# Optimization experiments

Measured on AMD Instinct MI355X. Metric: run time of the kernel, lower is better.

Reference implementation:

```python
import jax, jax.numpy as jnp
import numpy as np
import math

B_ = 4
L_ = 2048
D_MODEL = 1024
D_STATE = 128
D_CONV = 4
HEADDIM = 64
CHUNK = 256
D_INNER = 2 * D_MODEL
NHEADS = D_INNER // HEADDIM
CONV_DIM = D_INNER + 2 * D_STATE
D_IN_PROJ = 2 * D_INNER + 2 * D_STATE + NHEADS


def setup_inputs() -> dict:
    key = jax.random.key(0)
    ks = jax.random.split(key, 8)
    u = jax.random.normal(ks[0], (B_, L_, D_MODEL), jnp.float32)
    W_in = jax.random.normal(ks[1], (D_IN_PROJ, D_MODEL), jnp.float32) * 0.02
    conv_w = jax.random.normal(ks[2], (CONV_DIM, D_CONV), jnp.float32) * 0.2
    conv_b = jnp.zeros((CONV_DIM,), jnp.float32)
    # dt init as in the torch module: dt ~ logU(0.001, 0.1), inverse-softplus
    dt = jnp.exp(jax.random.uniform(ks[3], (NHEADS,), jnp.float32) * (math.log(0.1) - math.log(0.001)) + math.log(0.001))
    dt = jnp.clip(dt, 1e-4, None)
    dt_bias = dt + jnp.log(-jnp.expm1(-dt))
    A_log = jnp.log(jax.random.uniform(ks[4], (NHEADS,), jnp.float32, minval=1.0, maxval=1.1))
    D_param = jnp.ones((NHEADS,), jnp.float32)
    norm_w = jnp.ones((D_INNER,), jnp.float32)
    W_out = jax.random.normal(ks[5], (D_MODEL, D_INNER), jnp.float32) * 0.02
    return {"u": u, "W_in": W_in, "conv_w": conv_w, "conv_b": conv_b,
            "dt_bias": dt_bias, "A_log": A_log, "D_param": D_param,
            "norm_w": norm_w, "W_out": W_out}


def _ssd(x, dt, A, Bm, Cm):
    """Chunked SSD scan (mamba_chunk_scan_combined math, ngroups=1).
    x: (b,l,h,p)  dt: (b,l,h) post-softplus  A: (h,)  Bm/Cm: (b,l,n)."""
    b, l, h, p = x.shape
    n = Bm.shape[-1]
    nc = l // CHUNK
    xr = x.reshape(b, nc, CHUNK, h, p)
    dtr = dt.reshape(b, nc, CHUNK, h)
    Br = Bm.reshape(b, nc, CHUNK, n)
    Cr = Cm.reshape(b, nc, CHUNK, n)
    dA = dtr * A                                    # (b,nc,cs,h), negative
    dA_cs = jnp.cumsum(dA, axis=2)                  # (b,nc,cs,h)
    # intra-chunk decay L[i,j] = exp(sum_{k=j+1..i} dA_k) for i >= j else 0
    diff = dA_cs[:, :, :, None, :] - dA_cs[:, :, None, :, :]  # (b,nc,i,j,h)
    mask = jnp.tril(jnp.ones((CHUNK, CHUNK), bool))
    Lmat = jnp.exp(jnp.where(mask[None, None, :, :, None], diff, -jnp.inf))
    dtx = dtr[..., None] * xr                       # (b,nc,cs,h,p)
    Y_diag = jnp.einsum('bcin,bcjn,bcijh,bcjhp->bcihp', Cr, Br, Lmat, dtx)
    # per-chunk final states
    decay_states = jnp.exp(dA_cs[:, :, -1:, :] - dA_cs)  # (b,nc,cs,h)
    states = jnp.einsum('bcjn,bcjh,bcjhp->bchpn', Br, decay_states, dtx)
    # inter-chunk recurrence over nc
    chunk_decay = jnp.exp(dA_cs[:, :, -1, :])       # (b,nc,h)
    def step(carry, inp):
        s, d = inp
        return carry * d[:, :, None, None] + s, carry
    init = jnp.zeros((b, h, p, n), x.dtype)
    _, prev = jax.lax.scan(step, init, (jnp.moveaxis(states, 1, 0), jnp.moveaxis(chunk_decay, 1, 0)))
    prev = jnp.moveaxis(prev, 0, 1)                 # (b,nc,h,p,n): state entering each chunk
    Y_off = jnp.einsum('bcin,bchpn,bcih->bcihp', Cr, prev, jnp.exp(dA_cs))
    return (Y_diag + Y_off).reshape(b, l, h, p)


def reference(u, W_in, conv_w, conv_b, dt_bias, A_log, D_param, norm_w, W_out):
    b, l, _ = u.shape
    zxbcdt = jnp.einsum('bld,ed->ble', u, W_in)     # (b,l,d_in_proj)
    z = zxbcdt[..., :D_INNER]
    xBC = zxbcdt[..., D_INNER:D_INNER + CONV_DIM]
    dt = zxbcdt[..., D_INNER + CONV_DIM:]
    # depthwise causal conv1d + SiLU
    xt = jnp.moveaxis(xBC, 1, 2)                    # (b,c,l)
    y = jax.lax.conv_general_dilated(xt, conv_w[:, None, :], (1,), [(D_CONV - 1, 0)], feature_group_count=CONV_DIM)
    xBC = jax.nn.silu(jnp.moveaxis(y + conv_b[None, :, None], 2, 1))
    x = xBC[..., :D_INNER].reshape(b, l, NHEADS, HEADDIM)
    Bm = xBC[..., D_INNER:D_INNER + D_STATE]
    Cm = xBC[..., D_INNER + D_STATE:]
    dt = jax.nn.softplus(dt + dt_bias)
    A = -jnp.exp(A_log)
    yh = _ssd(x, dt, A, Bm, Cm) + D_param[:, None] * x
    yf = yh.reshape(b, l, D_INNER)
    # gated RMSNorm (norm_before_gate=False): norm(y * silu(z)) * w
    g = yf * jax.nn.silu(z)
    g = g * jax.lax.rsqrt(jnp.mean(g * g, axis=-1, keepdims=True) + 1e-5) * norm_w
    return jnp.einsum('bld,ed->ble', g, W_out)
```

## Files before the change

kernel.cpp:

```cpp
#include <hip/hip_runtime.h>
#include <hip/hip_bf16.h>
#include <math.h>

#define B_N     4
#define L_N     2048
#define DMODEL  1024
#define DSTATE  128
#define DCONV   4
#define HEADDIM 64
#define CHUNK   256
#define DINNER  2048
#define NHEADS  32
#define CONVDIM 2304
#define DINPROJ 4384
#define NCHUNK  8
#define BL      (B_N*L_N)

typedef unsigned short ushort_t;
typedef unsigned int   uint_t;

typedef __attribute__((ext_vector_type(8))) short bf16x8;
typedef __attribute__((ext_vector_type(4))) float f32x4;

__device__ __forceinline__ float bfbits2f(ushort_t u){
    union { uint_t i; float f; } v; v.i = ((uint_t)u) << 16; return v.f;
}
__device__ __forceinline__ ushort_t f2bf(float f){
    union { float f; uint_t i; } v; v.f = f;
    uint_t r = v.i + 0x7FFF + ((v.i >> 16) & 1);
    return (ushort_t)(r >> 16);
}
__device__ __forceinline__ void gload_lds16(const void* g, void* l){
    __builtin_amdgcn_global_load_lds(
        (const __attribute__((address_space(1))) unsigned int*)g,
        (__attribute__((address_space(3))) unsigned int*)l, 16, 0, 0);
}

__global__ __launch_bounds__(256) void cvt_bf16(
    const float* __restrict__ in, ushort_t* __restrict__ out, int n8)
{
    int i = blockIdx.x*256 + threadIdx.x;
    if (i >= n8) return;
    const float4* p = (const float4*)(in + (size_t)i*8);
    float4 a = p[0], b = p[1];
    ushort_t o[8] = { f2bf(a.x), f2bf(a.y), f2bf(a.z), f2bf(a.w),
                      f2bf(b.x), f2bf(b.y), f2bf(b.z), f2bf(b.w) };
    *(uint4*)(out + (size_t)i*8) = *(const uint4*)o;
}

__global__ __launch_bounds__(256) void cvt_wT(
    const float* __restrict__ cw, float* __restrict__ wT)
{
    int c = blockIdx.x*256 + threadIdx.x;
    if (c >= CONVDIM) return;
    float4 v = *(const float4*)&cw[c*DCONV];
    wT[0*CONVDIM + c] = v.x;
    wT[1*CONVDIM + c] = v.y;
    wT[2*CONVDIM + c] = v.z;
    wT[3*CONVDIM + c] = v.w;
}

template<int KDIM, int NTILES, int EPI>
__global__ __launch_bounds__(256) void gemm_bt_mfma(
    const ushort_t* __restrict__ A, const ushort_t* __restrict__ B,
    float* __restrict__ outf, ushort_t* __restrict__ z, ushort_t* __restrict__ xbc,
    const float* __restrict__ dt_bias, float* __restrict__ dtp)
{
    __shared__ __align__(16) ushort_t Asl[2][128*32];
    __shared__ __align__(16) ushort_t Bsl[2][128*32];

    int nwg = gridDim.x;
    int cpx = nwg >> 3;
    int lin = blockIdx.x;
    int work = (lin & 7)*cpx + (lin >> 3);
    int mtile = work / NTILES, ntile = work % NTILES;
    int m0 = mtile*128, n0 = ntile*128;

    int t = threadIdx.x;
    int l = t & 63, w = t >> 6;
    int wr = w >> 1, wc = w & 1;
    int lr16 = l & 15, kb = l >> 4;
    int srow = t >> 2, skc = (t & 3)*8;

    f32x4 acc[4][4];
    #pragma unroll
    for (int m=0;m<4;m++){
        #pragma unroll
        for (int n=0;n<4;n++) acc[m][n] = (f32x4){0.f,0.f,0.f,0.f};
    }

    int br0 = n0 + srow, br1 = n0 + 64 + srow;
    if (EPI == 1){
        br0 = (br0 < DINPROJ) ? br0 : (DINPROJ-1);
        br1 = (br1 < DINPROJ) ? br1 : (DINPROJ-1);
    }

    auto stage = [&](int buf, int k0){
        gload_lds16(A + (size_t)(m0+srow)*KDIM + k0 + skc,    &Asl[buf][t*8]);
        gload_lds16(A + (size_t)(m0+64+srow)*KDIM + k0 + skc, &Asl[buf][2048 + t*8]);
        gload_lds16(B + (size_t)br0*KDIM + k0 + skc,          &Bsl[buf][t*8]);
        gload_lds16(B + (size_t)br1*KDIM + k0 + skc,          &Bsl[buf][2048 + t*8]);
    };

    auto compute = [&](int cur){
        bf16x8 af[4], bfr[4];
        #pragma unroll
        for (int m=0;m<4;m++) af[m]  = *(const bf16x8*)&Asl[cur][(wr*64+m*16+lr16)*32 + kb*8];
        #pragma unroll
        for (int n=0;n<4;n++) bfr[n] = *(const bf16x8*)&Bsl[cur][(wc*64+n*16+lr16)*32 + kb*8];
        __builtin_amdgcn_s_setprio(1);
        #pragma unroll
        for (int m=0;m<4;m++){
            #pragma unroll
            for (int n=0;n<4;n++)
                acc[m][n] = __builtin_amdgcn_mfma_f32_16x16x32_bf16(af[m], bfr[n], acc[m][n], 0, 0, 0);
        }
        __builtin_amdgcn_s_setprio(0);
    };

    stage(0, 0);
    __syncthreads();
    int cur = 0;

    for (int k0=32; k0<KDIM; k0+=32){
        stage(cur^1, k0);
        compute(cur);
        __syncthreads();
        cur ^= 1;
    }
    compute(cur);

    #pragma unroll
    for (int m=0;m<4;m++){
        int rbase = m0 + wr*64 + m*16 + (l>>4)*4;
        #pragma unroll
        for (int n=0;n<4;n++){
            int gcol = n0 + wc*64 + n*16 + lr16;
            f32x4 v = acc[m][n];
            #pragma unroll
            for (int q=0;q<4;q++){
                int row = rbase + q;
                if (EPI == 0) {
                    outf[(size_t)row*DMODEL + gcol] = v[q];
                } else {
                    if (gcol < DINNER) {
                        z[(size_t)row*DINNER + gcol] = f2bf(v[q]);
                    } else if (gcol < DINNER + CONVDIM) {
                        xbc[(size_t)row*CONVDIM + (gcol - DINNER)] = f2bf(v[q]);
                    } else if (gcol < DINPROJ) {
                        int hh = gcol - (DINNER + CONVDIM);
                        float x = v[q] + dt_bias[hh];
                        float sp = (x > 15.f) ? x : log1pf(__expf(x));
                        int bb = row >> 11, ll = row & (L_N-1);
                        dtp[((size_t)bb*NHEADS + hh)*L_N + ll] = sp;
                    }
                }
            }
        }
    }
}

__global__ __launch_bounds__(256) void conv_silu(
    const __hip_bfloat16* __restrict__ xraw,
    const float* __restrict__ wT, const float* __restrict__ cb,
    __hip_bfloat16* __restrict__ xout)
{
    int idx = blockIdx.x*256 + threadIdx.x;
    int c8 = (idx % (CONVDIM/8))*8;
    int ml = idx / (CONVDIM/8);
    int b  = ml >> 11, l = ml & (L_N-1);
    const ushort_t* xr = (const ushort_t*)xraw;
    float acc[8];
    {
        float4 b0 = *(const float4*)&cb[c8];
        float4 b1 = *(const float4*)&cb[c8+4];
        acc[0]=b0.x; acc[1]=b0.y; acc[2]=b0.z; acc[3]=b0.w;
        acc[4]=b1.x; acc[5]=b1.y; acc[6]=b1.z; acc[7]=b1.w;
    }
    #pragma unroll
    for (int k=0;k<DCONV;k++){
        int li = l - (DCONV-1) + k;
        if (li >= 0){
            bf16x8 v = *(const bf16x8*)&xr[((size_t)b*L_N + li)*CONVDIM + c8];
            float4 w0 = *(const float4*)&wT[k*CONVDIM + c8];
            float4 w1 = *(const float4*)&wT[k*CONVDIM + c8 + 4];
            float wv[8] = {w0.x,w0.y,w0.z,w0.w,w1.x,w1.y,w1.z,w1.w};
            #pragma unroll
            for (int e=0;e<8;e++)
                acc[e] += wv[e] * bfbits2f(((const ushort_t*)&v)[e]);
        }
    }
    ushort_t o[8];
    #pragma unroll
    for (int e=0;e<8;e++){
        float s = acc[e] / (1.f + __expf(-acc[e]));
        o[e] = f2bf(s);
    }
    *(uint4*)((ushort_t*)xout + (size_t)idx*8) = *(const uint4*)o;
}

__global__ __launch_bounds__(256) void dt_cumsum(
    const float* __restrict__ dtp, const float* __restrict__ A_log,
    float* __restrict__ dAcs)
{
    int blk = blockIdx.x;
    int c  = blk % NCHUNK;
    int bh = blk / NCHUNK;
    int h  = bh & (NHEADS-1);
    int t  = threadIdx.x;
    float A = -__expf(A_log[h]);
    __shared__ float sm[CHUNK];
    float v = dtp[(size_t)bh*L_N + c*CHUNK + t] * A;
    sm[t] = v;
    __syncthreads();
    for (int off=1; off<CHUNK; off<<=1){
        float add = (t >= off) ? sm[t-off] : 0.f;
        __syncthreads();
        sm[t] += add;
        __syncthreads();
    }
    dAcs[(size_t)bh*L_N + c*CHUNK + t] = sm[t];
}

__global__ __launch_bounds__(256) void bc_scores_mfma(
    const __hip_bfloat16* __restrict__ xbc, ushort_t* __restrict__ S_T)
{
    __shared__ __align__(16) ushort_t Bs2[256*136];
    __shared__ __align__(16) ushort_t Cs2[256*136];
    int bc = blockIdx.x;
    int t = threadIdx.x;
    int l = t & 63, w = t >> 6;
    int l15 = l & 15, l4 = l >> 4;
    const ushort_t* xb = (const ushort_t*)xbc;
    const size_t rowbase = (size_t)bc*CHUNK*CONVDIM;

    #pragma unroll
    for (int ps=0; ps<16; ps++){
        int idx = ps*256 + t;
        int r = idx >> 4, ck = idx & 15;
        *(uint4*)&Bs2[r*136 + ck*8] =
            *(const uint4*)&xb[rowbase + (size_t)r*CONVDIM + DINNER + ck*8];
        *(uint4*)&Cs2[r*136 + ck*8] =
            *(const uint4*)&xb[rowbase + (size_t)r*CONVDIM + (DINNER+DSTATE) + ck*8];
    }
    __syncthreads();

    ushort_t* Sb = S_T + (size_t)bc*CHUNK*264;
    for (int if4 = w; if4 < 4; if4++){
        f32x4 acc[4][4];
        #pragma unroll
        for (int jf=0;jf<4;jf++){
            #pragma unroll
            for (int ir=0;ir<4;ir++) acc[jf][ir] = (f32x4){0.f,0.f,0.f,0.f};
        }
        #pragma unroll
        for (int k=0;k<4;k++){
            bf16x8 af[4], bfC[4];
            #pragma unroll
            for (int jf=0;jf<4;jf++)
                af[jf] = *(const bf16x8*)&Bs2[(w*64 + jf*16 + l15)*136 + k*32 + l4*8];
            #pragma unroll
            for (int ir=0;ir<4;ir++)
                bfC[ir] = *(const bf16x8*)&Cs2[(if4*64 + ir*16 + l15)*136 + k*32 + l4*8];
            #pragma unroll
            for (int jf=0;jf<4;jf++){
                #pragma unroll
                for (int ir=0;ir<4;ir++)
                    acc[jf][ir] = __builtin_amdgcn_mfma_f32_16x16x32_bf16(af[jf], bfC[ir], acc[jf][ir], 0, 0, 0);
            }
        }
        #pragma unroll
        for (int jf=0;jf<4;jf++){
            #pragma unroll
            for (int ir=0;ir<4;ir++){
                #pragma unroll
                for (int q=0;q<4;q++){
                    int j = w*64 + jf*16 + l4*4 + q;
                    int i = if4*64 + ir*16 + l15;
                    Sb[(size_t)j*264 + i] = f2bf(acc[jf][ir][q]);
                }
            }
        }
    }
}

__device__ __forceinline__ int swz264(int row, int col){
    return row*264 + (col ^ (((row>>3)&7)<<3));
}

__global__ __launch_bounds__(256) void ssd_states_mfma(
    const __hip_bfloat16* __restrict__ xbc,
    const float* __restrict__ dtp, const float* __restrict__ dAcs,
    float* __restrict__ states)
{
    __shared__ __align__(16) ushort_t xdT[64*264];
    __shared__ __align__(16) ushort_t BT[128*264];
    __shared__ float coef_s[CHUNK];
    int bc = blockIdx.x, h = blockIdx.y;
    int b = bc >> 3, c = bc & 7;
    int t = threadIdx.x;
    int l = t & 63, w = t >> 6;
    int l15 = l & 15, l4 = l >> 4;
    const ushort_t* xb = (const ushort_t*)xbc;
    const size_t rowbase = (size_t)bc*CHUNK*CONVDIM;

    size_t dbase = ((size_t)b*NHEADS + h)*L_N + c*CHUNK;
    float last = dAcs[dbase + CHUNK-1];
    coef_s[t] = __expf(last - dAcs[dbase + t]) * dtp[dbase + t];
    __syncthreads();

    #pragma unroll
    for (int ps=0; ps<8; ps++){
        int idx = ps*256 + t;
        int j = idx >> 3, p0 = (idx & 7)*8;
        float cj = coef_s[j];
        bf16x8 v = *(const bf16x8*)&xb[rowbase + (size_t)j*CONVDIM + h*HEADDIM + p0];
        #pragma unroll
        for (int e=0;e<8;e++)
            xdT[swz264(p0+e, j)] = f2bf(cj * bfbits2f(((const ushort_t*)&v)[e]));
    }
    #pragma unroll
    for (int ps=0; ps<16; ps++){
        int idx = ps*256 + t;
        int j = idx >> 4, n0 = (idx & 15)*8;
        bf16x8 v = *(const bf16x8*)&xb[rowbase + (size_t)j*CONVDIM + DINNER + n0];
        #pragma unroll
        for (int e=0;e<8;e++)
            BT[swz264(n0+e, j)] = ((const ushort_t*)&v)[e];
    }
    __syncthreads();

    f32x4 acc[4][2];
    #pragma unroll
    for (int pf=0;pf<4;pf++){
        #pragma unroll
        for (int nf=0;nf<2;nf++) acc[pf][nf] = (f32x4){0.f,0.f,0.f,0.f};
    }

    #pragma unroll
    for (int k=0;k<8;k++){
        bf16x8 af[4], bv[2];
        #pragma unroll
        for (int pf=0;pf<4;pf++)
            af[pf] = *(const bf16x8*)&xdT[swz264(pf*16 + l15, k*32 + l4*8)];
        #pragma unroll
        for (int nf=0;nf<2;nf++)
            bv[nf] = *(const bf16x8*)&BT[swz264(w*32 + nf*16 + l15, k*32 + l4*8)];
        #pragma unroll
        for (int pf=0;pf<4;pf++){
            #pragma unroll
            for (int nf=0;nf<2;nf++)
                acc[pf][nf] = __builtin_amdgcn_mfma_f32_16x16x32_bf16(af[pf], bv[nf], acc[pf][nf], 0, 0, 0);
        }
    }

    float* sb = states + (size_t)(bc*NHEADS + h)*HEADDIM*DSTATE;
    #pragma unroll
    for (int pf=0;pf<4;pf++){
        #pragma unroll
        for (int nf=0;nf<2;nf++){
            #pragma unroll
            for (int q=0;q<4;q++){
                int p = pf*16 + l4*4 + q;
                int n = w*32 + nf*16 + l15;
                sb[(size_t)p*DSTATE + n] = acc[pf][nf][q];
            }
        }
    }
}

__global__ __launch_bounds__(256) void scan_states(
    float* __restrict__ states, const float* __restrict__ dAcs)
{
    int idx = blockIdx.x*256 + threadIdx.x;
    int n  = idx & 127;
    int p  = (idx >> 7) & 63;
    int bh = idx >> 13;
    int b  = bh >> 5, h = bh & 31;
    float carry = 0.f;
    for (int c=0;c<NCHUNK;c++){
        size_t off = (((size_t)((b*NCHUNK + c)*NHEADS + h))*HEADDIM + p)*DSTATE + n;
        float s = states[off];
        states[off] = carry;
        float cd = __expf(dAcs[((size_t)b*NHEADS + h)*L_N + c*CHUNK + (CHUNK-1)]);
        carry = carry * cd + s;
    }
}

__global__ __launch_bounds__(256, 1) void ssd_mfma(
    const __hip_bfloat16* __restrict__ xbc,
    const float* __restrict__ dtp, const float* __restrict__ dAcs,
    const float* __restrict__ states, const ushort_t* __restrict__ S_T,
    const float* __restrict__ D_param, float* __restrict__ yh)
{
    __shared__ __align__(16) ushort_t Cs[256*136];
    __shared__ __align__(16) ushort_t Bs[64*136];
    __shared__ __align__(16) ushort_t Ws[256*72];
    __shared__ __align__(16) ushort_t xdT[64*264];
    __shared__ float da_s[CHUNK];
    __shared__ float dt_s[CHUNK];

    int bc = blockIdx.x, h = blockIdx.y;
    int b = bc >> 3, c = bc & 7;
    int t = threadIdx.x;
    int l = t & 63, w = t >> 6;
    int l15 = l & 15, l4 = l >> 4;

    const ushort_t* xb = (const ushort_t*)xbc;
    const size_t rowbase = (size_t)bc*CHUNK*CONVDIM;

    da_s[t] = dAcs[((size_t)b*NHEADS + h)*L_N + c*CHUNK + t];
    dt_s[t] = dtp[((size_t)b*NHEADS + h)*L_N + c*CHUNK + t];

    #pragma unroll
    for (int ps=0; ps<16; ps++){
        int idx = ps*256 + t;
        int r = idx >> 4, ck = idx & 15;
        *(uint4*)&Cs[r*136 + ck*8] =
            *(const uint4*)&xb[rowbase + (size_t)r*CONVDIM + (DINNER+DSTATE) + ck*8];
    }
    #pragma unroll
    for (int ps=0; ps<8; ps++){
        int idx = ps*256 + t;
        int j = idx >> 3, p0 = (idx & 7)*8;
        bf16x8 v = *(const bf16x8*)&xb[rowbase + (size_t)j*CONVDIM + h*HEADDIM + p0];
        #pragma unroll
        for (int e=0;e<8;e++) xdT[(p0+e)*264 + j] = ((const ushort_t*)&v)[e];
    }
    const float* sbp = states + (size_t)(bc*NHEADS + h)*HEADDIM*DSTATE;
    #pragma unroll
    for (int ps=0; ps<8; ps++){
        int idx = ps*256 + t;
        int p = idx >> 5, n0 = (idx & 31)*4;
        float4 v = *(const float4*)&sbp[p*DSTATE + n0];
        ushort_t o[4] = { f2bf(v.x), f2bf(v.y), f2bf(v.z), f2bf(v.w) };
        *(uint2*)&Bs[p*136 + n0] = *(const uint2*)o;
    }
    __syncthreads();

    f32x4 yacc[4][4];
    #pragma unroll
    for (int m=0;m<4;m++){
        #pragma unroll
        for (int np=0;np<4;np++) yacc[m][np] = (f32x4){0.f,0.f,0.f,0.f};
    }

    #pragma unroll
    for (int k=0;k<4;k++){
        bf16x8 bfk[4];
        #pragma unroll
        for (int np=0;np<4;np++)
            bfk[np] = *(const bf16x8*)&Bs[(np*16 + l15)*136 + k*32 + l4*8];
        #pragma unroll
        for (int m=0;m<4;m++){
            int i0 = (m*4 + w)*16;
            bf16x8 af = *(const bf16x8*)&Cs[(i0 + l15)*136 + k*32 + l4*8];
            #pragma unroll
            for (int np=0;np<4;np++)
                yacc[m][np] = __builtin_amdgcn_mfma_f32_16x16x32_bf16(af, bfk[np], yacc[m][np], 0, 0, 0);
        }
    }
    #pragma unroll
    for (int m=0;m<4;m++){
        int i0 = (m*4 + w)*16;
        #pragma unroll
        for (int q=0;q<4;q++){
            float e = __expf(da_s[i0 + l4*4 + q]);
            #pragma unroll
            for (int np=0;np<4;np++) yacc[m][np][q] *= e;
        }
    }

    const ushort_t* Sb = S_T + (size_t)bc*CHUNK*264;
    for (int jp=0; jp<4; jp++){
        bf16x8 bfx[4][2];
        #pragma unroll
        for (int np=0;np<4;np++){
            #pragma unroll
            for (int ks=0;ks<2;ks++)
                bfx[np][ks] = *(const bf16x8*)&xdT[(np*16 + l15)*264 + jp*64 + ks*32 + l4*8];
        }

        #pragma unroll
        for (int m=0;m<4;m++){
            int i0 = (m*4 + w)*16;
            int imax = i0 + 15;
            int kmaxY = (jp*64 <= imax ? 1 : 0) + (jp*64+32 <= imax ? 1 : 0);
            if (kmaxY == 0) continue;
            int nmax = 2*kmaxY;

            float dai[4];
            #pragma unroll
            for (int q=0;q<4;q++) dai[q] = da_s[i0 + l4*4 + q];
            #pragma unroll
            for (int n=0;n<4;n++){
                if (n < nmax){
                    int jcol = jp*64 + n*16 + l15;
                    float daj = da_s[jcol], dtj = dt_s[jcol];
                    ushort_t sv[4];
                    *(uint2*)sv = *(const uint2*)&Sb[(size_t)jcol*264 + i0 + l4*4];
                    #pragma unroll
                    for (int q=0;q<4;q++){
                        int i = i0 + l4*4 + q;
                        float wv = 0.f;
                        if (jcol <= i) wv = __expf(dai[q] - daj) * dtj * bfbits2f(sv[q]);
                        Ws[i*72 + n*16 + l15] = f2bf(wv);
                    }
                }
            }
            #pragma unroll
            for (int ks=0;ks<2;ks++){
                if (ks < kmaxY){
                    bf16x8 wfA = *(const bf16x8*)&Ws[(i0 + l15)*72 + ks*32 + l4*8];
                    #pragma unroll
                    for (int np=0;np<4;np++)
                        yacc[m][np] = __builtin_amdgcn_mfma_f32_16x16x32_bf16(wfA, bfx[np][ks], yacc[m][np], 0, 0, 0);
                }
            }
        }
    }

    float Dh = D_param[h];
    #pragma unroll
    for (int m=0;m<4;m++){
        int i0 = (m*4 + w)*16;
        #pragma unroll
        for (int np=0;np<4;np++){
            int p = np*16 + l15;
            #pragma unroll
            for (int q=0;q<4;q++){
                int i = i0 + l4*4 + q;
                float xv = bfbits2f(xdT[p*264 + i]);
                yh[((size_t)bc*CHUNK + i)*DINNER + h*HEADDIM + p] = yacc[m][np][q] + Dh*xv;
            }
        }
    }
}

__global__ __launch_bounds__(256) void gate_norm(
    const float* __restrict__ yh, const __hip_bfloat16* __restrict__ z,
    const float* __restrict__ norm_w, __hip_bfloat16* __restrict__ g)
{
    int row = blockIdx.x;
    int t = threadIdx.x;
    const float* yr = yh + (size_t)row*DINNER;
    const ushort_t* zr = (const ushort_t*)z + (size_t)row*DINNER;
    float v[8];
    float ss = 0.f;
    #pragma unroll
    for (int r=0;r<8;r++){
        int d = r*256 + t;
        float zv = bfbits2f(zr[d]);
        float gv = yr[d] * (zv / (1.f + __expf(-zv)));
        v[r] = gv; ss += gv*gv;
    }
    #pragma unroll
    for (int off=32; off>=1; off>>=1) ss += __shfl_xor(ss, off);
    __shared__ float red[4];
    if ((t & 63) == 0) red[t >> 6] = ss;
    __syncthreads();
    float tot = red[0]+red[1]+red[2]+red[3];
    float scale = rsqrtf(tot * (1.f/DINNER) + 1e-5f);
    __hip_bfloat16* gr = g + (size_t)row*DINNER;
    #pragma unroll
    for (int r=0;r<8;r++){
        int d = r*256 + t;
        gr[d] = __float2bfloat16(v[r]*scale*norm_w[d]);
    }
}

extern "C" void kernel_launch(void* const* d_in, const int* in_sizes, int n_in,
                              void* d_out, int out_size, void* d_ws, size_t ws_size,
                              hipStream_t stream)
{
    const float* u       = (const float*)d_in[0];
    const float* W_in    = (const float*)d_in[1];
    const float* conv_w  = (const float*)d_in[2];
    const float* conv_b  = (const float*)d_in[3];
    const float* dt_bias = (const float*)d_in[4];
    const float* A_log   = (const float*)d_in[5];
    const float* D_param = (const float*)d_in[6];
    const float* norm_w  = (const float*)d_in[7];
    const float* W_out   = (const float*)d_in[8];
    float* out = (float*)d_out;

    char* p = (char*)d_ws;
    auto take = [&](size_t n){ char* r = p; p += (n + 255) & ~(size_t)255; return r; };

    __hip_bfloat16* z       = (__hip_bfloat16*)take((size_t)BL*DINNER*2);
    __hip_bfloat16* xbc_raw = (__hip_bfloat16*)take((size_t)BL*CONVDIM*2);
    __hip_bfloat16* xbc     = (__hip_bfloat16*)take((size_t)BL*CONVDIM*2);
    float* dtp     = (float*)take((size_t)BL*NHEADS*4);
    float* dAcs    = (float*)take((size_t)BL*NHEADS*4);
    float* states  = (float*)take((size_t)B_N*NCHUNK*NHEADS*HEADDIM*DSTATE*4);
    float* yh      = (float*)take((size_t)BL*DINNER*4);
    ushort_t* S_T  = (ushort_t*)take((size_t)B_N*NCHUNK*CHUNK*264*2);
    ushort_t* u_bf  = (ushort_t*)take((size_t)BL*DMODEL*2);
    ushort_t* Wi_bf = (ushort_t*)take((size_t)DINPROJ*DMODEL*2);
    ushort_t* Wo_bf = (ushort_t*)take((size_t)DMODEL*DINNER*2);
    float* wT       = (float*)take((size_t)DCONV*CONVDIM*4);
    __hip_bfloat16* g = z;

    cvt_bf16<<<dim3((BL*DMODEL/8 + 255)/256), 256, 0, stream>>>(u, u_bf, BL*DMODEL/8);
    cvt_bf16<<<dim3((DINPROJ*DMODEL/8 + 255)/256), 256, 0, stream>>>(W_in, Wi_bf, DINPROJ*DMODEL/8);
    cvt_bf16<<<dim3((DMODEL*DINNER/8 + 255)/256), 256, 0, stream>>>(W_out, Wo_bf, DMODEL*DINNER/8);
    cvt_wT<<<dim3((CONVDIM+255)/256), 256, 0, stream>>>(conv_w, wT);

    gemm_bt_mfma<DMODEL,35,1><<<dim3(64*35), 256, 0, stream>>>(
        u_bf, Wi_bf, nullptr, (ushort_t*)z, (ushort_t*)xbc_raw, dt_bias, dtp);

    conv_silu<<<dim3(BL*(CONVDIM/8)/256), 256, 0, stream>>>(xbc_raw, wT, conv_b, xbc);
    dt_cumsum<<<dim3(B_N*NHEADS*NCHUNK), 256, 0, stream>>>(dtp, A_log, dAcs);
    bc_scores_mfma<<<dim3(B_N*NCHUNK), 256, 0, stream>>>(xbc, S_T);
    ssd_states_mfma<<<dim3(B_N*NCHUNK, NHEADS), 256, 0, stream>>>(xbc, dtp, dAcs, states);
    scan_states<<<dim3((B_N*NHEADS*HEADDIM*DSTATE)/256), 256, 0, stream>>>(states, dAcs);
    ssd_mfma<<<dim3(B_N*NCHUNK, NHEADS), 256, 0, stream>>>(xbc, dtp, dAcs, states, S_T, D_param, yh);
    gate_norm<<<dim3(BL), 256, 0, stream>>>(yh, z, norm_w, g);

    gemm_bt_mfma<DINNER,8,0><<<dim3(64*8), 256, 0, stream>>>(
        (const ushort_t*)g, Wo_bf, out, nullptr, nullptr, nullptr, nullptr);
}
```

Baseline: 399.9 us.

## Batch heads in state kernel, drop LDS staging, store yh as bf16

ssd_states_mfma now processes four heads per block and reuses the staged B transpose across them, which cuts the number of B loads into shared memory by four. ssd_mfma no longer stages C and the chunk states in shared memory. It reads MFMA fragments straight from global memory, converting states to bf16 in registers, and drops the one-block-per-CU launch bound so occupancy can rise. The yh intermediate becomes bf16, halving its write and read traffic, and gate_norm is vectorised to match. The trade-offs are fewer blocks for the state kernel, uncoalesced global fragment reads, and lower precision for yh.

```diff
diff --git a/kernel.cpp b/kernel.cpp
--- a/kernel.cpp
+++ b/kernel.cpp
@@ -296,7 +296,7 @@
     __shared__ __align__(16) ushort_t xdT[64*264];
     __shared__ __align__(16) ushort_t BT[128*264];
     __shared__ float coef_s[CHUNK];
-    int bc = blockIdx.x, h = blockIdx.y;
+    int bc = blockIdx.x, hg = blockIdx.y;
     int b = bc >> 3, c = bc & 7;
     int t = threadIdx.x;
     int l = t & 63, w = t >> 6;
@@ -304,21 +304,6 @@
     const ushort_t* xb = (const ushort_t*)xbc;
     const size_t rowbase = (size_t)bc*CHUNK*CONVDIM;
 
-    size_t dbase = ((size_t)b*NHEADS + h)*L_N + c*CHUNK;
-    float last = dAcs[dbase + CHUNK-1];
-    coef_s[t] = __expf(last - dAcs[dbase + t]) * dtp[dbase + t];
-    __syncthreads();
-
-    #pragma unroll
-    for (int ps=0; ps<8; ps++){
-        int idx = ps*256 + t;
-        int j = idx >> 3, p0 = (idx & 7)*8;
-        float cj = coef_s[j];
-        bf16x8 v = *(const bf16x8*)&xb[rowbase + (size_t)j*CONVDIM + h*HEADDIM + p0];
-        #pragma unroll
-        for (int e=0;e<8;e++)
-            xdT[swz264(p0+e, j)] = f2bf(cj * bfbits2f(((const ushort_t*)&v)[e]));
-    }
     #pragma unroll
     for (int ps=0; ps<16; ps++){
         int idx = ps*256 + t;
@@ -328,42 +313,62 @@
         for (int e=0;e<8;e++)
             BT[swz264(n0+e, j)] = ((const ushort_t*)&v)[e];
     }
-    __syncthreads();
-
-    f32x4 acc[4][2];
-    #pragma unroll
-    for (int pf=0;pf<4;pf++){
-        #pragma unroll
-        for (int nf=0;nf<2;nf++) acc[pf][nf] = (f32x4){0.f,0.f,0.f,0.f};
-    }
-
-    #pragma unroll
-    for (int k=0;k<8;k++){
-        bf16x8 af[4], bv[2];
-        #pragma unroll
-        for (int pf=0;pf<4;pf++)
-            af[pf] = *(const bf16x8*)&xdT[swz264(pf*16 + l15, k*32 + l4*8)];
-        #pragma unroll
-        for (int nf=0;nf<2;nf++)
-            bv[nf] = *(const bf16x8*)&BT[swz264(w*32 + nf*16 + l15, k*32 + l4*8)];
+
+    for (int hh=0; hh<4; hh++){
+        int h = hg*4 + hh;
+        size_t dbase = ((size_t)b*NHEADS + h)*L_N + c*CHUNK;
+        float last = dAcs[dbase + CHUNK-1];
+        float cf = __expf(last - dAcs[dbase + t]) * dtp[dbase + t];
+        coef_s[t] = cf;
+        __syncthreads();
+
+        #pragma unroll
+        for (int ps=0; ps<8; ps++){
+            int idx = ps*256 + t;
+            int j = idx >> 3, p0 = (idx & 7)*8;
+            float cj = coef_s[j];
+            bf16x8 v = *(const bf16x8*)&xb[rowbase + (size_t)j*CONVDIM + h*HEADDIM + p0];
+            #pragma unroll
+            for (int e=0;e<8;e++)
+                xdT[swz264(p0+e, j)] = f2bf(cj * bfbits2f(((const ushort_t*)&v)[e]));
+        }
+        __syncthreads();
+
+        f32x4 acc[4][2];
         #pragma unroll
         for (int pf=0;pf<4;pf++){
             #pragma unroll
+            for (int nf=0;nf<2;nf++) acc[pf][nf] = (f32x4){0.f,0.f,0.f,0.f};
+        }
+
+        #pragma unroll
+        for (int k=0;k<8;k++){
+            bf16x8 af[4], bv[2];
+            #pragma unroll
+            for (int pf=0;pf<4;pf++)
+                af[pf] = *(const bf16x8*)&xdT[swz264(pf*16 + l15, k*32 + l4*8)];
+            #pragma unroll
             for (int nf=0;nf<2;nf++)
-                acc[pf][nf] = __builtin_amdgcn_mfma_f32_16x16x32_bf16(af[pf], bv[nf], acc[pf][nf], 0, 0, 0);
-        }
-    }
-
-    float* sb = states + (size_t)(bc*NHEADS + h)*HEADDIM*DSTATE;
-    #pragma unroll
-    for (int pf=0;pf<4;pf++){
-        #pragma unroll
-        for (int nf=0;nf<2;nf++){
-            #pragma unroll
-            for (int q=0;q<4;q++){
-                int p = pf*16 + l4*4 + q;
-                int n = w*32 + nf*16 + l15;
-                sb[(size_t)p*DSTATE + n] = acc[pf][nf][q];
+                bv[nf] = *(const bf16x8*)&BT[swz264(w*32 + nf*16 + l15, k*32 + l4*8)];
+            #pragma unroll
+            for (int pf=0;pf<4;pf++){
+                #pragma unroll
+                for (int nf=0;nf<2;nf++)
+                    acc[pf][nf] = __builtin_amdgcn_mfma_f32_16x16x32_bf16(af[pf], bv[nf], acc[pf][nf], 0, 0, 0);
+            }
+        }
+
+        float* sb = states + (size_t)(bc*NHEADS + h)*HEADDIM*DSTATE;
+        #pragma unroll
+        for (int pf=0;pf<4;pf++){
+            #pragma unroll
+            for (int nf=0;nf<2;nf++){
+                #pragma unroll
+                for (int q=0;q<4;q++){
+                    int p = pf*16 + l4*4 + q;
+                    int n = w*32 + nf*16 + l15;
+                    sb[(size_t)p*DSTATE + n] = acc[pf][nf][q];
+                }
             }
         }
     }
@@ -387,14 +392,12 @@
     }
 }
 
-__global__ __launch_bounds__(256, 1) void ssd_mfma(
+__global__ __launch_bounds__(256) void ssd_mfma(
     const __hip_bfloat16* __restrict__ xbc,
     const float* __restrict__ dtp, const float* __restrict__ dAcs,
     const float* __restrict__ states, const ushort_t* __restrict__ S_T,
-    const float* __restrict__ D_param, float* __restrict__ yh)
-{
-    __shared__ __align__(16) ushort_t Cs[256*136];
-    __shared__ __align__(16) ushort_t Bs[64*136];
+    const float* __restrict__ D_param, ushort_t* __restrict__ yh)
+{
     __shared__ __align__(16) ushort_t Ws[256*72];
     __shared__ __align__(16) ushort_t xdT[64*264];
     __shared__ float da_s[CHUNK];
@@ -413,13 +416,6 @@
     dt_s[t] = dtp[((size_t)b*NHEADS + h)*L_N + c*CHUNK + t];
 
     #pragma unroll
-    for (int ps=0; ps<16; ps++){
-        int idx = ps*256 + t;
-        int r = idx >> 4, ck = idx & 15;
-        *(uint4*)&Cs[r*136 + ck*8] =
-            *(const uint4*)&xb[rowbase + (size_t)r*CONVDIM + (DINNER+DSTATE) + ck*8];
-    }
-    #pragma unroll
     for (int ps=0; ps<8; ps++){
         int idx = ps*256 + t;
         int j = idx >> 3, p0 = (idx & 7)*8;
@@ -427,15 +423,6 @@
         #pragma unroll
         for (int e=0;e<8;e++) xdT[(p0+e)*264 + j] = ((const ushort_t*)&v)[e];
     }
-    const float* sbp = states + (size_t)(bc*NHEADS + h)*HEADDIM*DSTATE;
-    #pragma unroll
-    for (int ps=0; ps<8; ps++){
-        int idx = ps*256 + t;
-        int p = idx >> 5, n0 = (idx & 31)*4;
-        float4 v = *(const float4*)&sbp[p*DSTATE + n0];
-        ushort_t o[4] = { f2bf(v.x), f2bf(v.y), f2bf(v.z), f2bf(v.w) };
-        *(uint2*)&Bs[p*136 + n0] = *(const uint2*)o;
-    }
     __syncthreads();
 
     f32x4 yacc[4][4];
@@ -445,16 +432,28 @@
         for (int np=0;np<4;np++) yacc[m][np] = (f32x4){0.f,0.f,0.f,0.f};
     }
 
+    const ushort_t* cbase = xb + rowbase + (size_t)l15*CONVDIM + (DINNER+DSTATE) + l4*8;
+    const float*    pbase = states + (size_t)(bc*NHEADS + h)*HEADDIM*DSTATE
+                                   + (size_t)l15*DSTATE + l4*8;
     #pragma unroll
     for (int k=0;k<4;k++){
         bf16x8 bfk[4];
         #pragma unroll
-        for (int np=0;np<4;np++)
-            bfk[np] = *(const bf16x8*)&Bs[(np*16 + l15)*136 + k*32 + l4*8];
+        for (int np=0;np<4;np++){
+            const float* pr = pbase + (size_t)(np*16)*DSTATE + k*32;
+            float4 a = *(const float4*)pr;
+            float4 bq = *(const float4*)(pr + 4);
+            bf16x8 r;
+            r[0]=(short)f2bf(a.x);  r[1]=(short)f2bf(a.y);
+            r[2]=(short)f2bf(a.z);  r[3]=(short)f2bf(a.w);
+            r[4]=(short)f2bf(bq.x); r[5]=(short)f2bf(bq.y);
+            r[6]=(short)f2bf(bq.z); r[7]=(short)f2bf(bq.w);
+            bfk[np] = r;
+        }
         #pragma unroll
         for (int m=0;m<4;m++){
             int i0 = (m*4 + w)*16;
-            bf16x8 af = *(const bf16x8*)&Cs[(i0 + l15)*136 + k*32 + l4*8];
+            bf16x8 af = *(const bf16x8*)(cbase + (size_t)i0*CONVDIM + k*32);
             #pragma unroll
             for (int np=0;np<4;np++)
                 yacc[m][np] = __builtin_amdgcn_mfma_f32_16x16x32_bf16(af, bfk[np], yacc[m][np], 0, 0, 0);
@@ -531,28 +530,30 @@
             for (int q=0;q<4;q++){
                 int i = i0 + l4*4 + q;
                 float xv = bfbits2f(xdT[p*264 + i]);
-                yh[((size_t)bc*CHUNK + i)*DINNER + h*HEADDIM + p] = yacc[m][np][q] + Dh*xv;
+                yh[((size_t)bc*CHUNK + i)*DINNER + h*HEADDIM + p] = f2bf(yacc[m][np][q] + Dh*xv);
             }
         }
     }
 }
 
 __global__ __launch_bounds__(256) void gate_norm(
-    const float* __restrict__ yh, const __hip_bfloat16* __restrict__ z,
+    const ushort_t* __restrict__ yh, const __hip_bfloat16* __restrict__ z,
     const float* __restrict__ norm_w, __hip_bfloat16* __restrict__ g)
 {
     int row = blockIdx.x;
     int t = threadIdx.x;
-    const float* yr = yh + (size_t)row*DINNER;
-    const ushort_t* zr = (const ushort_t*)z + (size_t)row*DINNER;
+    const ushort_t* yr = yh + (size_t)row*DINNER + t*8;
+    const ushort_t* zr = (const ushort_t*)z + (size_t)row*DINNER + t*8;
+    bf16x8 yv = *(const bf16x8*)yr;
+    bf16x8 zv8 = *(const bf16x8*)zr;
     float v[8];
     float ss = 0.f;
     #pragma unroll
-    for (int r=0;r<8;r++){
-        int d = r*256 + t;
-        float zv = bfbits2f(zr[d]);
-        float gv = yr[d] * (zv / (1.f + __expf(-zv)));
-        v[r] = gv; ss += gv*gv;
+    for (int e=0;e<8;e++){
+        float y = bfbits2f(((const ushort_t*)&yv)[e]);
+        float zz = bfbits2f(((const ushort_t*)&zv8)[e]);
+        float gv = y * (zz / (1.f + __expf(-zz)));
+        v[e] = gv; ss += gv*gv;
     }
     #pragma unroll
     for (int off=32; off>=1; off>>=1) ss += __shfl_xor(ss, off);
@@ -561,12 +562,13 @@
     __syncthreads();
     float tot = red[0]+red[1]+red[2]+red[3];
     float scale = rsqrtf(tot * (1.f/DINNER) + 1e-5f);
-    __hip_bfloat16* gr = g + (size_t)row*DINNER;
-    #pragma unroll
-    for (int r=0;r<8;r++){
-        int d = r*256 + t;
-        gr[d] = __float2bfloat16(v[r]*scale*norm_w[d]);
-    }
+    float4 w0 = *(const float4*)&norm_w[t*8];
+    float4 w1 = *(const float4*)&norm_w[t*8+4];
+    float nw[8] = {w0.x,w0.y,w0.z,w0.w,w1.x,w1.y,w1.z,w1.w};
+    ushort_t o[8];
+    #pragma unroll
+    for (int e=0;e<8;e++) o[e] = f2bf(v[e]*scale*nw[e]);
+    *(uint4*)((ushort_t*)g + (size_t)row*DINNER + t*8) = *(const uint4*)o;
 }
 
 extern "C" void kernel_launch(void* const* d_in, const int* in_sizes, int n_in,
@@ -593,7 +595,7 @@
     float* dtp     = (float*)take((size_t)BL*NHEADS*4);
     float* dAcs    = (float*)take((size_t)BL*NHEADS*4);
     float* states  = (float*)take((size_t)B_N*NCHUNK*NHEADS*HEADDIM*DSTATE*4);
-    float* yh      = (float*)take((size_t)BL*DINNER*4);
+    ushort_t* yh   = (ushort_t*)take((size_t)BL*DINNER*2);
     ushort_t* S_T  = (ushort_t*)take((size_t)B_N*NCHUNK*CHUNK*264*2);
     ushort_t* u_bf  = (ushort_t*)take((size_t)BL*DMODEL*2);
     ushort_t* Wi_bf = (ushort_t*)take((size_t)DINPROJ*DMODEL*2);
@@ -612,7 +614,7 @@
     conv_silu<<<dim3(BL*(CONVDIM/8)/256), 256, 0, stream>>>(xbc_raw, wT, conv_b, xbc);
     dt_cumsum<<<dim3(B_N*NHEADS*NCHUNK), 256, 0, stream>>>(dtp, A_log, dAcs);
     bc_scores_mfma<<<dim3(B_N*NCHUNK), 256, 0, stream>>>(xbc, S_T);
-    ssd_states_mfma<<<dim3(B_N*NCHUNK, NHEADS), 256, 0, stream>>>(xbc, dtp, dAcs, states);
+    ssd_states_mfma<<<dim3(B_N*NCHUNK, NHEADS/4), 256, 0, stream>>>(xbc, dtp, dAcs, states);
     scan_states<<<dim3((B_N*NHEADS*HEADDIM*DSTATE)/256), 256, 0, stream>>>(states, dAcs);
     ssd_mfma<<<dim3(B_N*NCHUNK, NHEADS), 256, 0, stream>>>(xbc, dtp, dAcs, states, S_T, D_param, yh);
     gate_norm<<<dim3(BL), 256, 0, stream>>>(yh, z, norm_w, g);
```

Result: faster. 366.5 us (-8.3%).
